# Kernel tuning notes

Measured on AMD Instinct MI355X. Metric: run time of the kernel, lower is better.

## Reference

```python
import jax, jax.numpy as jnp
import numpy as np

MAXLEN = 30
VOCAB_SIZE = 20000
THOUGHT = 1200
WORD = 620
BATCH = 130  # decoder uses B-2 = 128 sequences


def setup_inputs() -> dict:
    key = jax.random.key(0)
    ks = jax.random.split(key, 8)
    s_ih = 1.0 / np.sqrt(WORD)
    return {
        "thoughts": jax.random.normal(ks[0], (BATCH, THOUGHT), dtype=jnp.float32),
        "embed_table": jax.random.normal(ks[1], (VOCAB_SIZE, WORD), dtype=jnp.float32),
        "W_ih": jax.random.uniform(ks[2], (4 * WORD, 2 * THOUGHT + WORD), jnp.float32, -s_ih, s_ih),
        "W_hh": jax.random.uniform(ks[3], (4 * WORD, WORD), jnp.float32, -s_ih, s_ih),
        "b_ih": jax.random.uniform(ks[4], (4 * WORD,), jnp.float32, -s_ih, s_ih),
        "b_hh": jax.random.uniform(ks[5], (4 * WORD,), jnp.float32, -s_ih, s_ih),
        "Ww": jax.random.uniform(ks[6], (VOCAB_SIZE, WORD), jnp.float32, -s_ih, s_ih),
        "bw": jax.random.uniform(ks[7], (VOCAB_SIZE,), jnp.float32, -s_ih, s_ih),
    }


def reference(thoughts, embed_table, W_ih, W_hh, b_ih, b_hh, Ww, bw):
    # context: concat(thoughts_prev, thoughts_next) -> [B-2, 2*THOUGHT]
    ctx = jnp.concatenate([thoughts[:-2], thoughts[2:]], axis=1)
    n = ctx.shape[0]
    h0 = jnp.zeros((n, WORD), dtype=thoughts.dtype)  # (h,c) reset to 0 each step

    def step(last_word, _):
        x = jnp.concatenate([ctx, last_word], axis=1)  # [n, 3020]
        # LSTM cell with zero initial state (original discards state each step)
        gates = x @ W_ih.T + b_ih + h0 @ W_hh.T + b_hh  # [n, 4*WORD]
        i, f, g, o = jnp.split(gates, 4, axis=1)
        c = jax.nn.sigmoid(i) * jnp.tanh(g)  # f-gate irrelevant, c_prev = 0
        h = jax.nn.sigmoid(o) * jnp.tanh(c)  # [n, WORD]
        logits = h @ Ww.T + bw               # [n, VOCAB]
        idx = jnp.argmax(logits, axis=1)
        new_last = embed_table[idx]          # greedy-decoded word embedding
        return new_last, h

    _, hs = jax.lax.scan(step, h0, None, length=MAXLEN)  # [MAXLEN, n, WORD]
    pred = jnp.einsum("tnw,vw->tnv", hs, Ww) + bw        # [MAXLEN, n, VOCAB]
    return jnp.transpose(pred, (1, 0, 2))                 # [n, MAXLEN, VOCAB]
```

## Files before the change

### kernel.cpp

```cpp
#include <hip/hip_runtime.h>
#include <math.h>

#define VOCAB 20000
#define WORD 620
#define NSEQ 128
#define TMAX 30
#define CTXK 2400
#define XK 3020
#define NBLK 256

typedef unsigned long long u64;
typedef __attribute__((ext_vector_type(8))) short short8;
typedef __attribute__((ext_vector_type(4))) float f32x4;

__device__ __forceinline__ unsigned ford(float f) {
    unsigned b = __float_as_uint(f);
    return (b & 0x80000000u) ? ~b : (b | 0x80000000u);
}
__device__ __forceinline__ unsigned short bf16rne(float x) {
    unsigned u = __float_as_uint(x);
    return (unsigned short)((u + 0x7fffu + ((u >> 16) & 1u)) >> 16);
}
__device__ __forceinline__ float bf16tof(unsigned short h) {
    return __uint_as_float(((unsigned)h) << 16);
}
__device__ __forceinline__ short8 ld8(const unsigned short* p) {
    return *(const short8*)p;
}
#define MFMA(a, b, c) __builtin_amdgcn_mfma_f32_16x16x32_bf16((a), (b), (c), 0, 0, 0)
#define VMW(N) asm volatile("s_waitcnt vmcnt(" #N ")" ::: "memory")
#define AL64(p) __hip_atomic_load((p), __ATOMIC_RELAXED, __HIP_MEMORY_SCOPE_AGENT)

__device__ __forceinline__ void gridbar(unsigned* bar, unsigned epoch, bool rel) {
    __syncthreads();
    if (threadIdx.x == 0) {
        if (rel) __threadfence();
        unsigned g = blockIdx.x >> 4;
        unsigned a = __hip_atomic_fetch_add(&bar[g * 16], 1u, __ATOMIC_RELAXED, __HIP_MEMORY_SCOPE_AGENT);
        if (a == epoch * 16u - 1u)
            __hip_atomic_fetch_add(&bar[256], 1u, __ATOMIC_RELAXED, __HIP_MEMORY_SCOPE_AGENT);
        while (__hip_atomic_load(&bar[256], __ATOMIC_RELAXED, __HIP_MEMORY_SCOPE_AGENT) < epoch * 16u)
            __builtin_amdgcn_s_sleep(2);
    }
    __syncthreads();
}


__global__ __launch_bounds__(256) void kpack_w(const float* __restrict__ src,
                                               unsigned short* __restrict__ dst,
                                               int nvt, int nks, int col0,
                                               int ncols_valid, int src_ld,
                                               int nrows_valid, int rowmap) {
    int i = blockIdx.x * 256 + threadIdx.x;
    if (i >= nvt * nks * 512) return;
    int j = i & 7;
    int lane = (i >> 3) & 63;
    int t2 = i >> 9;
    int ks = t2 % nks;
    int vt = t2 / nks;
    int r = vt * 16 + (lane & 15);
    int k = ks * 32 + ((lane >> 4) << 3) + j;
    float x = 0.f;
    if (r < nrows_valid && k < ncols_valid) {
        int row = (rowmap == 1) ? ((r < 620) ? r : r + 620) : r;
        x = src[(size_t)row * src_ld + col0 + k];
    }
    unsigned short hi = bf16rne(x);
    unsigned short lo = bf16rne(x - bf16tof(hi));
    size_t ob = (size_t)t2 * 1024 + lane * 8 + j;
    dst[ob] = hi;
    dst[ob + 512] = lo;
}

__global__ __launch_bounds__(256) void kpack_ctx(const float* __restrict__ th,
                                                 unsigned short* __restrict__ dst) {
    int i = blockIdx.x * 256 + threadIdx.x;
    if (i >= 75 * 8 * 512) return;
    int j = i & 7;
    int lane = (i >> 3) & 63;
    int t2 = i >> 9;
    int mt = t2 & 7;
    int ks = t2 >> 3;
    int n = mt * 16 + (lane & 15);
    int k = ks * 32 + ((lane >> 4) << 3) + j;
    float x = (k < 1200) ? th[(size_t)n * 1200 + k]
                         : th[(size_t)(n + 2) * 1200 + (k - 1200)];
    unsigned short hi = bf16rne(x);
    unsigned short lo = bf16rne(x - bf16tof(hi));
    size_t ob = (size_t)t2 * 1024 + lane * 8 + j;
    dst[ob] = hi;
    dst[ob + 512] = lo;
}

__global__ __launch_bounds__(256) void kpack_embed(const float* __restrict__ embed,
                                                   unsigned short* __restrict__ ehi,
                                                   unsigned short* __restrict__ elo) {
    size_t i = (size_t)blockIdx.x * 256 + threadIdx.x;
    if (i >= (size_t)VOCAB * 640) return;
    int v = (int)(i / 640);
    int k = (int)(i % 640);
    float x = (k < WORD) ? embed[(size_t)v * WORD + k] : 0.f;
    unsigned short hi = bf16rne(x);
    ehi[i] = hi;
    elo[i] = bf16rne(x - bf16tof(hi));
}

__global__ __launch_bounds__(256) void ggemm(const unsigned short* __restrict__ Af,
                                             const unsigned short* __restrict__ Bf,
                                             const float* __restrict__ addRow,
                                             const float* __restrict__ addFull,
                                             float* __restrict__ outT,
                                             int nks, int nvt, int ldout) {
    int lane = threadIdx.x & 63, wv = threadIdx.x >> 6;
    int vtb = blockIdx.x * 8 + wv * 2;
    bool ok0 = vtb < nvt, ok1 = (vtb + 1) < nvt;
    f32x4 acc[8][2];
#pragma unroll
    for (int m = 0; m < 8; ++m) { acc[m][0] = (f32x4)0.f; acc[m][1] = (f32x4)0.f; }
    if (ok0) {
        const unsigned short* ap = Af + lane * 8;
        const unsigned short* bp0 = Bf + (size_t)vtb * nks * 1024 + lane * 8;
        const unsigned short* bp1 = bp0 + (size_t)nks * 1024;
        for (int ks = 0; ks < nks; ++ks) {
            short8 b0h = ld8(bp0), b0l = ld8(bp0 + 512);
            short8 ah[8], al[8];
#pragma unroll
            for (int m = 0; m < 8; ++m) {
                ah[m] = ld8(ap + m * 1024);
                al[m] = ld8(ap + m * 1024 + 512);
            }
#pragma unroll
            for (int m = 0; m < 8; ++m) {
                acc[m][0] = MFMA(ah[m], b0h, acc[m][0]);
                acc[m][0] = MFMA(ah[m], b0l, acc[m][0]);
                acc[m][0] = MFMA(al[m], b0h, acc[m][0]);
            }
            if (ok1) {
                short8 b1h = ld8(bp1), b1l = ld8(bp1 + 512);
#pragma unroll
                for (int m = 0; m < 8; ++m) {
                    acc[m][1] = MFMA(ah[m], b1h, acc[m][1]);
                    acc[m][1] = MFMA(ah[m], b1l, acc[m][1]);
                    acc[m][1] = MFMA(al[m], b1h, acc[m][1]);
                }
            }
            ap += 8192; bp0 += 1024; bp1 += 1024;
        }
    }
    int rbase = (lane >> 4) << 2;
    int cof = lane & 15;
#pragma unroll
    for (int v = 0; v < 2; ++v) {
        bool ok = v ? ok1 : ok0;
        if (!ok) continue;
        int col = (vtb + v) * 16 + cof;
        float ar = addRow ? addRow[col] : 0.f;
#pragma unroll
        for (int m = 0; m < 8; ++m) {
#pragma unroll
            for (int r = 0; r < 4; ++r) {
                int row = m * 16 + rbase + r;
                float x = acc[m][v][r] + ar;
                if (addFull) x += addFull[(size_t)row * ldout + col];
                outT[(size_t)row * ldout + col] = x;
            }
        }
    }
}

__global__ __launch_bounds__(256) void kinit3(unsigned* hf32, unsigned* slots32,
                                              float* bsum, unsigned* bar,
                                              const float* __restrict__ b_ih,
                                              const float* __restrict__ b_hh) {
    int i = blockIdx.x * 256 + threadIdx.x;
    if (i < 81920) hf32[i] = 0u;
    if (i < 7680) slots32[i] = 0u;
    if (i < 512) bar[i] = 0u;
    if (i < 1872) {
        float v = 0.f;
        if (i < 1860) {
            int row = (i < 620) ? i : i + 620;
            v = b_ih[row] + b_hh[row];
        }
        bsum[i] = v;
    }
}

__global__ __launch_bounds__(512, 2) void kmega(
    const unsigned short* __restrict__ embhi,
    const unsigned short* __restrict__ emblo,
    const unsigned short* __restrict__ Wgf3,
    const unsigned short* __restrict__ Wwf,
    const float* __restrict__ base,
    const float* __restrict__ bw,
    unsigned short* __restrict__ hf,
    u64* __restrict__ slots,
    float* __restrict__ out,
    unsigned* bar) {
    __shared__ char sA[3][16384];
    __shared__ u64 keybuf[128];
    const int tid = threadIdx.x;
    const int lane = tid & 63;
    const int wv = tid >> 6;
    const int bid = blockIdx.x;

    const int vt_lo = (int)(((long long)bid * 1250) / NBLK);
    const int vt_hi = (int)(((long long)(bid + 1) * 1250) / NBLK);
    const int nvt = vt_hi - vt_lo;
    const bool act = (wv < nvt);
    const int myvt = vt_lo + (act ? wv : 0);
    const bool gact = (bid < 39);

    const char* hfb = (const char*)hf;
    const unsigned short* Bbase = Wwf + (size_t)myvt * 20480 + lane * 8;
    unsigned epoch = 0;

    u64 R[2][4];
    short8 Bh[3], Bl[3];

#define ISSUE(M)                                                               \
    do {                                                                       \
        const u64* ga_ = (const u64*)(hfb + (size_t)(M) * 16384 +              \
                                      wv * 2048 + lane * 16);                  \
        R[(M) & 1][0] = AL64(ga_ + 0);                                         \
        R[(M) & 1][1] = AL64(ga_ + 1);                                         \
        R[(M) & 1][2] = AL64(ga_ + 128);                                       \
        R[(M) & 1][3] = AL64(ga_ + 129);                                       \
        if (act) {                                                             \
            const unsigned short* bp_ = Bbase + (size_t)(M) * 1024;            \
            Bh[(M) % 3] = ld8(bp_);                                            \
            Bl[(M) % 3] = ld8(bp_ + 512);                                      \
        }                                                                      \
    } while (0)

#define WRA(M)                                                                 \
    do {                                                                       \
        u64* da_ = (u64*)(sA[(M) % 3] + wv * 2048 + lane * 16);                \
        da_[0] = R[(M) & 1][0];                                                \
        da_[1] = R[(M) & 1][1];                                                \
        da_[128] = R[(M) & 1][2];                                              \
        da_[129] = R[(M) & 1][3];                                              \
    } while (0)

#define LSTEP(K)                                                               \
    do {                                                                       \
        if ((K) + 2 < 20) ISSUE((K) + 2);                                      \
        if ((K) <= 17) { if (act) { VMW(6); } else { VMW(4); } }               \
        else { VMW(0); }                                                       \
        if ((K) + 1 < 20) WRA((K) + 1);                                        \
        asm volatile("s_waitcnt lgkmcnt(0)" ::: "memory");                     \
        __builtin_amdgcn_s_barrier();                                          \
        __builtin_amdgcn_sched_barrier(0);                                     \
        if (act) {                                                             \
            const unsigned short* ab_ = (const unsigned short*)sA[(K) % 3];    \
            _Pragma("unroll")                                                  \
            for (int mt = 0; mt < 8; ++mt) {                                   \
                short8 ah_ = ld8(ab_ + mt * 1024 + lane * 8);                  \
                short8 al_ = ld8(ab_ + mt * 1024 + 512 + lane * 8);            \
                acc[mt] = MFMA(ah_, Bh[(K) % 3], acc[mt]);                     \
                acc[mt] = MFMA(ah_, Bl[(K) % 3], acc[mt]);                     \
                acc[mt] = MFMA(al_, Bh[(K) % 3], acc[mt]);                     \
            }                                                                  \
        }                                                                      \
    } while (0)

    for (int t = 0; t < TMAX; ++t) {
        if (gact) {
            const int g_vt = bid;
            const int g_mt = wv;
            f32x4 aI = (f32x4)0.f, aG = (f32x4)0.f, aO = (f32x4)0.f;
            if (t > 0) {
                int n = g_mt * 16 + (lane & 15);
                u64 s = AL64(&slots[(size_t)(t - 1) * NSEQ + n]);
                unsigned idx = 0xFFFFFFFFu - (unsigned)(s & 0xFFFFFFFFull);
                const unsigned short* eh = embhi + (size_t)idx * 640 + ((lane >> 4) << 3);
                const unsigned short* el = emblo + (size_t)idx * 640 + ((lane >> 4) << 3);
                const unsigned short* bI = Wgf3 + (size_t)(0 * 39 + g_vt) * 20480 + lane * 8;
                const unsigned short* bG = Wgf3 + (size_t)(1 * 39 + g_vt) * 20480 + lane * 8;
                const unsigned short* bO = Wgf3 + (size_t)(2 * 39 + g_vt) * 20480 + lane * 8;
#pragma unroll 2
                for (int ks = 0; ks < 20; ++ks) {
                    short8 ah = ld8(eh + ks * 32);
                    short8 al = ld8(el + ks * 32);
                    short8 bIh = ld8(bI), bIl = ld8(bI + 512);
                    short8 bGh = ld8(bG), bGl = ld8(bG + 512);
                    short8 bOh = ld8(bO), bOl = ld8(bO + 512);
                    aI = MFMA(ah, bIh, aI); aI = MFMA(ah, bIl, aI); aI = MFMA(al, bIh, aI);
                    aG = MFMA(ah, bGh, aG); aG = MFMA(ah, bGl, aG); aG = MFMA(al, bGh, aG);
                    aO = MFMA(ah, bOh, aO); aO = MFMA(ah, bOl, aO); aO = MFMA(al, bOh, aO);
                    bI += 1024; bG += 1024; bO += 1024;
                }
            }
            int col = g_vt * 16 + (lane & 15);
            if (col < WORD) {
                int rbase = g_mt * 16 + ((lane >> 4) << 2);
#pragma unroll
                for (int r = 0; r < 4; ++r) {
                    int n = rbase + r;
                    float gi = aI[r] + base[(size_t)n * 1872 + col];
                    float gg = aG[r] + base[(size_t)n * 1872 + 620 + col];
                    float go = aO[r] + base[(size_t)n * 1872 + 1240 + col];
                    float si = 1.f / (1.f + expf(-gi));
                    float so = 1.f / (1.f + expf(-go));
                    float h = so * tanhf(si * tanhf(gg));
                    int pos = (((col >> 5) * 8 + (n >> 4)) * 1024) +
                              (((n & 15) + (((col & 31) >> 3) << 4)) * 8) + (col & 7);
                    unsigned short hi = bf16rne(h);
                    hf[pos] = hi;
                    hf[pos + 512] = bf16rne(h - bf16tof(hi));
                }
            }
        }
        if (tid < 128) keybuf[tid] = 0ull;
        ++epoch;
        gridbar(bar, epoch, gact);

        f32x4 acc[8];
#pragma unroll
        for (int mt = 0; mt < 8; ++mt) acc[mt] = (f32x4)0.f;

        ISSUE(0);
        ISSUE(1);
        if (act) { VMW(6); } else { VMW(4); }
        WRA(0);

        LSTEP(0);  LSTEP(1);  LSTEP(2);  LSTEP(3);  LSTEP(4);
        LSTEP(5);  LSTEP(6);  LSTEP(7);  LSTEP(8);  LSTEP(9);
        LSTEP(10); LSTEP(11); LSTEP(12); LSTEP(13); LSTEP(14);
        LSTEP(15); LSTEP(16); LSTEP(17); LSTEP(18); LSTEP(19);

        int q = lane >> 4, cof = lane & 15;
        if (act) {
            int v = myvt * 16 + cof;
            float bwv = bw[v];
#pragma unroll
            for (int mt = 0; mt < 8; ++mt) {
#pragma unroll
                for (int r = 0; r < 4; ++r) {
                    int n = mt * 16 + q * 4 + r;
                    float x = acc[mt][r] + bwv;
                    out[((size_t)n * TMAX + t) * VOCAB + v] = x;
                    u64 key = ((u64)ford(x) << 32) | (u64)(0xFFFFFFFFu - (unsigned)v);
#pragma unroll
                    for (int s2 = 1; s2 <= 8; s2 <<= 1) {
                        u64 o = __shfl_xor(key, s2, 64);
                        if (o > key) key = o;
                    }
                    if (cof == 0) atomicMax(&keybuf[n], key);
                }
            }
        }
        __syncthreads();
        if (tid < 128) {
            u64 k = keybuf[tid];
            if (k) atomicMax(&slots[(size_t)t * NSEQ + tid], k);
        }
        if (t + 1 < TMAX) {
            ++epoch;
            gridbar(bar, epoch, false);
        }
    }
#undef LSTEP
#undef WRA
#undef ISSUE
}

__global__ __launch_bounds__(256) void kinit2(unsigned int* lastfrag32,
                                              unsigned int* hfrag32,
                                              unsigned int* slots32,
                                              float* bsum,
                                              const float* __restrict__ b_ih,
                                              const float* __restrict__ b_hh) {
    int i = blockIdx.x * 256 + threadIdx.x;
    if (i < 81920) { lastfrag32[i] = 0u; hfrag32[i] = 0u; }
    if (i < 7680) slots32[i] = 0u;
    if (i < 1872) {
        float v = 0.f;
        if (i < 1860) {
            int row = (i < 620) ? i : i + 620;
            v = b_ih[row] + b_hh[row];
        }
        bsum[i] = v;
    }
}

__global__ __launch_bounds__(256) void klogits2(const unsigned short* __restrict__ Hf,
                                                const unsigned short* __restrict__ Wf,
                                                const float* __restrict__ bw,
                                                float* __restrict__ out,
                                                u64* __restrict__ slots, int t) {
    __shared__ u64 keybuf[128];
    int tid = threadIdx.x;
    if (tid < 128) keybuf[tid] = 0ull;
    __syncthreads();
    int lane = tid & 63, wv = tid >> 6;
    int vtb = blockIdx.x * 8 + wv * 2;
    bool ok0 = vtb < 1250, ok1 = (vtb + 1) < 1250;
    f32x4 acc[8][2];
#pragma unroll
    for (int m = 0; m < 8; ++m) { acc[m][0] = (f32x4)0.f; acc[m][1] = (f32x4)0.f; }
    if (ok0) {
        const unsigned short* ap = Hf + lane * 8;
        const unsigned short* bp0 = Wf + (size_t)vtb * 20 * 1024 + lane * 8;
        const unsigned short* bp1 = bp0 + 20 * 1024;
#pragma unroll 2
        for (int ks = 0; ks < 20; ++ks) {
            short8 b0h = ld8(bp0), b0l = ld8(bp0 + 512);
            short8 ah[8], al[8];
#pragma unroll
            for (int m = 0; m < 8; ++m) {
                ah[m] = ld8(ap + m * 1024);
                al[m] = ld8(ap + m * 1024 + 512);
            }
#pragma unroll
            for (int m = 0; m < 8; ++m) {
                acc[m][0] = MFMA(ah[m], b0h, acc[m][0]);
                acc[m][0] = MFMA(ah[m], b0l, acc[m][0]);
                acc[m][0] = MFMA(al[m], b0h, acc[m][0]);
            }
            if (ok1) {
                short8 b1h = ld8(bp1), b1l = ld8(bp1 + 512);
#pragma unroll
                for (int m = 0; m < 8; ++m) {
                    acc[m][1] = MFMA(ah[m], b1h, acc[m][1]);
                    acc[m][1] = MFMA(ah[m], b1l, acc[m][1]);
                    acc[m][1] = MFMA(al[m], b1h, acc[m][1]);
                }
            }
            ap += 8192; bp0 += 1024; bp1 += 1024;
        }
    }
    int rbase = (lane >> 4) << 2;
    int cof = lane & 15;
    float bw0 = ok0 ? bw[vtb * 16 + cof] : 0.f;
    float bw1 = ok1 ? bw[(vtb + 1) * 16 + cof] : 0.f;
#pragma unroll
    for (int m = 0; m < 8; ++m) {
#pragma unroll
        for (int r = 0; r < 4; ++r) {
            int row = m * 16 + rbase + r;
            u64 km = 0ull;
            if (ok0) {
                int v = vtb * 16 + cof;
                float x = acc[m][0][r] + bw0;
                out[((size_t)row * TMAX + t) * VOCAB + v] = x;
                km = ((u64)ford(x) << 32) | (u64)(0xFFFFFFFFu - (unsigned)v);
            }
            if (ok1) {
                int v = (vtb + 1) * 16 + cof;
                float x = acc[m][1][r] + bw1;
                out[((size_t)row * TMAX + t) * VOCAB + v] = x;
                u64 k2 = ((u64)ford(x) << 32) | (u64)(0xFFFFFFFFu - (unsigned)v);
                if (k2 > km) km = k2;
            }
#pragma unroll
            for (int s2 = 1; s2 <= 8; s2 <<= 1) {
                u64 o = __shfl_xor(km, s2, 64);
                if (o > km) km = o;
            }
            if ((lane & 15) == 0 && km) atomicMax(&keybuf[row], km);
        }
    }
    __syncthreads();
    if (tid < 128) atomicMax(&slots[(size_t)t * NSEQ + tid], keybuf[tid]);
}

__global__ void kact(const float* __restrict__ gates,
                     unsigned short* __restrict__ hfrag) {
    int n = blockIdx.x;
    int k = threadIdx.x;
    if (k >= WORD) return;
    const float* g = gates + (size_t)n * 1872;
    float gi = g[k], gg = g[620 + k], go = g[1240 + k];
    float si = 1.f / (1.f + expf(-gi));
    float so = 1.f / (1.f + expf(-go));
    float h = so * tanhf(si * tanhf(gg));
    int ks = k >> 5, mt = n >> 4;
    int lane = (n & 15) + (((k & 31) >> 3) << 4);
    int j = k & 7;
    size_t ob = (size_t)(ks * 8 + mt) * 1024 + lane * 8 + j;
    unsigned short hi = bf16rne(h);
    hfrag[ob] = hi;
    hfrag[ob + 512] = bf16rne(h - bf16tof(hi));
}

__global__ void kgather2(const float* __restrict__ embed,
                         const u64* __restrict__ slots,
                         unsigned short* __restrict__ lastfrag, int t) {
    int n = blockIdx.x;
    int k = threadIdx.x;
    if (k >= WORD) return;
    u64 s = slots[(size_t)t * NSEQ + n];
    unsigned idx = 0xFFFFFFFFu - (unsigned)(s & 0xFFFFFFFFull);
    float x = embed[(size_t)idx * WORD + k];
    int ks = k >> 5, mt = n >> 4;
    int lane = (n & 15) + (((k & 31) >> 3) << 4);
    int j = k & 7;
    size_t ob = (size_t)(ks * 8 + mt) * 1024 + lane * 8 + j;
    unsigned short hi = bf16rne(x);
    lastfrag[ob] = hi;
    lastfrag[ob + 512] = bf16rne(x - bf16tof(hi));
}

extern "C" void kernel_launch(void* const* d_in, const int* in_sizes, int n_in,
                              void* d_out, int out_size, void* d_ws, size_t ws_size,
                              hipStream_t stream) {
    const float* thoughts = (const float*)d_in[0];
    const float* embed    = (const float*)d_in[1];
    const float* W_ih     = (const float*)d_in[2];
    const float* b_ih     = (const float*)d_in[4];
    const float* b_hh     = (const float*)d_in[5];
    const float* Ww       = (const float*)d_in[6];
    const float* bw       = (const float*)d_in[7];
    float* out = (float*)d_out;
    char* ws = (char*)d_ws;

    const size_t OFF_WWF  = 0;
    const size_t OFF_WBF  = 51200000;
    const size_t OFF_WGF3 = 69171200;
    const size_t OFF_CTXF = 73963520;
    const size_t OFF_EHI  = 75192320;
    const size_t OFF_ELO  = 100792320;
    const size_t OFF_HF   = 126392320;
    const size_t OFF_BASE = 126720000;
    const size_t OFF_BSUM = 127678464;
    const size_t OFF_SLOT = 127685952;
    const size_t OFF_BAR  = 127716672;
    const size_t NEED_MEGA = 127718720;

    if (ws_size >= NEED_MEGA) {
        unsigned short* Wwf  = (unsigned short*)(ws + OFF_WWF);
        unsigned short* Wbf  = (unsigned short*)(ws + OFF_WBF);
        unsigned short* Wgf3 = (unsigned short*)(ws + OFF_WGF3);
        unsigned short* ctxf = (unsigned short*)(ws + OFF_CTXF);
        unsigned short* ehi  = (unsigned short*)(ws + OFF_EHI);
        unsigned short* elo  = (unsigned short*)(ws + OFF_ELO);
        unsigned short* hf   = (unsigned short*)(ws + OFF_HF);
        float* base = (float*)(ws + OFF_BASE);
        float* bsum = (float*)(ws + OFF_BSUM);
        u64*   slots = (u64*)(ws + OFF_SLOT);
        unsigned* bar = (unsigned*)(ws + OFF_BAR);

        kinit3<<<320, 256, 0, stream>>>((unsigned*)hf, (unsigned*)slots, bsum, bar, b_ih, b_hh);
        kpack_w<<<50000, 256, 0, stream>>>(Ww, Wwf, 1250, 20, 0, 620, WORD, VOCAB, 0);
        kpack_w<<<17550, 256, 0, stream>>>(W_ih, Wbf, 117, 75, 0, 2400, XK, 1860, 1);
        kpack_w<<<1560, 256, 0, stream>>>(W_ih + (size_t)0 * XK,    Wgf3 + 0 * 798720, 39, 20, 2400, 620, XK, 620, 0);
        kpack_w<<<1560, 256, 0, stream>>>(W_ih + (size_t)1240 * XK, Wgf3 + 1 * 798720, 39, 20, 2400, 620, XK, 620, 0);
        kpack_w<<<1560, 256, 0, stream>>>(W_ih + (size_t)1860 * XK, Wgf3 + 2 * 798720, 39, 20, 2400, 620, XK, 620, 0);
        kpack_ctx<<<1200, 256, 0, stream>>>(thoughts, ctxf);
        kpack_embed<<<50000, 256, 0, stream>>>(embed, ehi, elo);
        ggemm<<<15, 256, 0, stream>>>(ctxf, Wbf, bsum, nullptr, base, 75, 117, 1872);

        kmega<<<NBLK, 512, 0, stream>>>(ehi, elo, Wgf3, Wwf, base, bw, hf, slots, out, bar);
    } else {
        const size_t F_WWF  = 0;
        const size_t F_WBF  = 51200000;
        const size_t F_WGF  = 69171200;
        const size_t F_CTXF = 73963520;
        const size_t F_HF   = 75192320;
        const size_t F_LF   = 75520000;
        const size_t F_BASE = 75847680;
        const size_t F_GATE = 76806144;
        const size_t F_BSUM = 77764608;
        const size_t F_SLOT = 77772096;

        unsigned short* Wwf  = (unsigned short*)(ws + F_WWF);
        unsigned short* Wbf  = (unsigned short*)(ws + F_WBF);
        unsigned short* Wgf  = (unsigned short*)(ws + F_WGF);
        unsigned short* ctxf = (unsigned short*)(ws + F_CTXF);
        unsigned short* hf   = (unsigned short*)(ws + F_HF);
        unsigned short* lf   = (unsigned short*)(ws + F_LF);
        float* base = (float*)(ws + F_BASE);
        float* gate = (float*)(ws + F_GATE);
        float* bsum = (float*)(ws + F_BSUM);
        u64*   slots = (u64*)(ws + F_SLOT);

        kinit2<<<320, 256, 0, stream>>>((unsigned int*)lf, (unsigned int*)hf,
                                        (unsigned int*)slots, bsum, b_ih, b_hh);
        kpack_w<<<50000, 256, 0, stream>>>(Ww, Wwf, 1250, 20, 0, 620, WORD, VOCAB, 0);
        kpack_w<<<17550, 256, 0, stream>>>(W_ih, Wbf, 117, 75, 0, 2400, XK, 1860, 1);
        kpack_w<<<4680, 256, 0, stream>>>(W_ih, Wgf, 117, 20, 2400, 620, XK, 1860, 1);
        kpack_ctx<<<1200, 256, 0, stream>>>(thoughts, ctxf);
        ggemm<<<15, 256, 0, stream>>>(ctxf, Wbf, bsum, nullptr, base, 75, 117, 1872);
        for (int t = 0; t < TMAX; ++t) {
            ggemm<<<15, 256, 0, stream>>>(lf, Wgf, nullptr, base, gate, 20, 117, 1872);
            kact<<<NSEQ, 640, 0, stream>>>(gate, hf);
            klogits2<<<157, 256, 0, stream>>>(hf, Wwf, bw, out, slots, t);
            if (t + 1 < TMAX)
                kgather2<<<NSEQ, 640, 0, stream>>>(embed, slots, lf, t);
        }
    }
}
```

Measured before the change: 1.771 ms.

## Keep Ww high-bf16 tiles resident in LDS across timesteps, deepen prefetch

Each block loads the high-bf16 half of its vocab tiles of Ww into a 100KB LDS buffer once, before the timestep loop, using global_load_lds. Inside the loop only the low half is still streamed from global memory, which roughly halves per-step weight traffic. The prefetch pipeline for the hidden-state A tiles and the low-half B tiles goes from two stages to three, with the vmcnt waits adjusted to match. Logits are now written with nontemporal stores so they do not pollute the cache. The cost is about 150KB of LDS per block, which rules out two blocks per CU, plus extra register buffers for the deeper pipeline.

```diff
diff --git a/kernel.cpp b/kernel.cpp
--- a/kernel.cpp
+++ b/kernel.cpp
@@ -30,6 +30,12 @@
 #define MFMA(a, b, c) __builtin_amdgcn_mfma_f32_16x16x32_bf16((a), (b), (c), 0, 0, 0)
 #define VMW(N) asm volatile("s_waitcnt vmcnt(" #N ")" ::: "memory")
 #define AL64(p) __hip_atomic_load((p), __ATOMIC_RELAXED, __HIP_MEMORY_SCOPE_AGENT)
+
+__device__ __forceinline__ void gload_lds16(const void* g, void* l) {
+    __builtin_amdgcn_global_load_lds((const __attribute__((address_space(1))) void*)g,
+                                     (__attribute__((address_space(3))) void*)l,
+                                     16, 0, 0);
+}
 
 __device__ __forceinline__ void gridbar(unsigned* bar, unsigned epoch, bool rel) {
     __syncthreads();
@@ -197,6 +203,7 @@
     u64* __restrict__ slots,
     float* __restrict__ out,
     unsigned* bar) {
+    __shared__ char sBhi[102400];
     __shared__ char sA[3][16384];
     __shared__ u64 keybuf[128];
     const int tid = threadIdx.x;
@@ -212,40 +219,45 @@
     const bool gact = (bid < 39);
 
     const char* hfb = (const char*)hf;
-    const unsigned short* Bbase = Wwf + (size_t)myvt * 20480 + lane * 8;
+    const char* wwb = (const char*)Wwf;
+    const unsigned short* BbaseLo = Wwf + (size_t)myvt * 20480 + 512 + lane * 8;
     unsigned epoch = 0;
 
-    u64 R[2][4];
-    short8 Bh[3], Bl[3];
+    for (int i = wv; i < nvt * 20; i += 8) {
+        const char* g = wwb + (size_t)(vt_lo + i / 20) * 40960 + (size_t)(i % 20) * 2048 + lane * 16;
+        gload_lds16(g, sBhi + (size_t)i * 1024);
+    }
+    VMW(0);
+    __syncthreads();
+
+    u64 R[3][4];
+    short8 Bl[4];
 
 #define ISSUE(M)                                                               \
     do {                                                                       \
         const u64* ga_ = (const u64*)(hfb + (size_t)(M) * 16384 +              \
                                       wv * 2048 + lane * 16);                  \
-        R[(M) & 1][0] = AL64(ga_ + 0);                                         \
-        R[(M) & 1][1] = AL64(ga_ + 1);                                         \
-        R[(M) & 1][2] = AL64(ga_ + 128);                                       \
-        R[(M) & 1][3] = AL64(ga_ + 129);                                       \
-        if (act) {                                                             \
-            const unsigned short* bp_ = Bbase + (size_t)(M) * 1024;            \
-            Bh[(M) % 3] = ld8(bp_);                                            \
-            Bl[(M) % 3] = ld8(bp_ + 512);                                      \
-        }                                                                      \
+        R[(M) % 3][0] = AL64(ga_ + 0);                                         \
+        R[(M) % 3][1] = AL64(ga_ + 1);                                         \
+        R[(M) % 3][2] = AL64(ga_ + 128);                                       \
+        R[(M) % 3][3] = AL64(ga_ + 129);                                       \
+        if (act) Bl[(M) % 4] = ld8(BbaseLo + (size_t)(M) * 1024);              \
     } while (0)
 
 #define WRA(M)                                                                 \
     do {                                                                       \
         u64* da_ = (u64*)(sA[(M) % 3] + wv * 2048 + lane * 16);                \
-        da_[0] = R[(M) & 1][0];                                                \
-        da_[1] = R[(M) & 1][1];                                                \
-        da_[128] = R[(M) & 1][2];                                              \
-        da_[129] = R[(M) & 1][3];                                              \
+        da_[0] = R[(M) % 3][0];                                                \
+        da_[1] = R[(M) % 3][1];                                                \
+        da_[128] = R[(M) % 3][2];                                              \
+        da_[129] = R[(M) % 3][3];                                              \
     } while (0)
 
 #define LSTEP(K)                                                               \
     do {                                                                       \
-        if ((K) + 2 < 20) ISSUE((K) + 2);                                      \
-        if ((K) <= 17) { if (act) { VMW(6); } else { VMW(4); } }               \
+        if ((K) + 3 < 20) ISSUE((K) + 3);                                      \
+        if ((K) <= 16) { if (act) { VMW(10); } else { VMW(8); } }              \
+        else if ((K) == 17) { if (act) { VMW(5); } else { VMW(4); } }          \
         else { VMW(0); }                                                       \
         if ((K) + 1 < 20) WRA((K) + 1);                                        \
         asm volatile("s_waitcnt lgkmcnt(0)" ::: "memory");                     \
@@ -253,13 +265,15 @@
         __builtin_amdgcn_sched_barrier(0);                                     \
         if (act) {                                                             \
             const unsigned short* ab_ = (const unsigned short*)sA[(K) % 3];    \
+            short8 bh_ = ld8((const unsigned short*)(sBhi +                    \
+                             (size_t)(wv * 20 + (K)) * 1024) + lane * 8);      \
             _Pragma("unroll")                                                  \
             for (int mt = 0; mt < 8; ++mt) {                                   \
                 short8 ah_ = ld8(ab_ + mt * 1024 + lane * 8);                  \
                 short8 al_ = ld8(ab_ + mt * 1024 + 512 + lane * 8);            \
-                acc[mt] = MFMA(ah_, Bh[(K) % 3], acc[mt]);                     \
-                acc[mt] = MFMA(ah_, Bl[(K) % 3], acc[mt]);                     \
-                acc[mt] = MFMA(al_, Bh[(K) % 3], acc[mt]);                     \
+                acc[mt] = MFMA(ah_, bh_, acc[mt]);                             \
+                acc[mt] = MFMA(ah_, Bl[(K) % 4], acc[mt]);                     \
+                acc[mt] = MFMA(al_, bh_, acc[mt]);                             \
             }                                                                  \
         }                                                                      \
     } while (0)
@@ -321,7 +335,8 @@
 
         ISSUE(0);
         ISSUE(1);
-        if (act) { VMW(6); } else { VMW(4); }
+        ISSUE(2);
+        if (act) { VMW(10); } else { VMW(8); }
         WRA(0);
 
         LSTEP(0);  LSTEP(1);  LSTEP(2);  LSTEP(3);  LSTEP(4);
@@ -339,7 +354,7 @@
                 for (int r = 0; r < 4; ++r) {
                     int n = mt * 16 + q * 4 + r;
                     float x = acc[mt][r] + bwv;
-                    out[((size_t)n * TMAX + t) * VOCAB + v] = x;
+                    __builtin_nontemporal_store(x, &out[((size_t)n * TMAX + t) * VOCAB + v]);
                     u64 key = ((u64)ford(x) << 32) | (u64)(0xFFFFFFFFu - (unsigned)v);
 #pragma unroll
                     for (int s2 = 1; s2 <= 8; s2 <<= 1) {
```

New measurement: 1.527 ms. 13.8% less time.
